# Performance work log

Hardware: AMD Instinct MI355X
Metric: run time of the kernel (lower is better)

## Reference

```python
import jax, jax.numpy as jnp
import numpy as np

IMG = 256      # image size implied by 8x8 grid * scale 32
THRE = 0.5
DIS = 4        # img_dislocate_size
B = 64


def _shift_map(s, size, dis):
    # Pixel-level coordinate map for the dislocated half: cell r starts at
    # max(r*s - dis, 0) (the torch while-loop clamps negative coords to 0).
    p = jnp.arange(size)
    base = jnp.maximum((p // s) * s - dis, 0)
    return base + p % s


def _cell_norm(x, g, s):
    # Per-cell (crop) min/max normalization, matching the per-crop
    # (t - min) / (max - min + 1e-5) in HeatMaptoImg.
    b = x.shape[0]
    v = x.reshape(b, 1, g, s, g, s)
    mn = v.min(axis=(3, 5), keepdims=True)
    mx = v.max(axis=(3, 5), keepdims=True)
    return ((v - mn) / (mx - mn + 1e-5)).reshape(b, 1, g * s, g * s)


def setup_inputs() -> dict:
    key = jax.random.key(0)
    ks = jax.random.split(key, 7)
    B2 = 2 * B
    return {
        "img": jax.random.uniform(ks[0], (B, 1, IMG, IMG), jnp.float32),
        "heat8": jax.random.uniform(ks[1], (B2, 1, 8, 8), jnp.float32),
        "heat16": jax.random.uniform(ks[2], (B2, 1, 16, 16), jnp.float32),
        "heat32": jax.random.uniform(ks[3], (B2, 1, 32, 32), jnp.float32),
        "seg8": jax.random.uniform(ks[4], (B2, 1, IMG, IMG), jnp.float32),
        "seg16": jax.random.uniform(ks[5], (B2, 1, IMG, IMG), jnp.float32),
        "seg32": jax.random.uniform(ks[6], (B2, 1, IMG, IMG), jnp.float32),
    }


def reference(img, heat8, heat16, heat32, seg8, seg16, seg32):
    Bv = img.shape[0]
    label = jnp.zeros((Bv, 1, IMG, IMG), img.dtype)
    cnt = jnp.zeros_like(label)
    crops = {}
    # fine grid (scale 8) processed first, matching the reversed loop order
    for heat, seg, g in ((heat32, seg32, 32), (heat16, seg16, 16), (heat8, seg8, 8)):
        s = IMG // g                      # crop / cell size for this scale
        mask = (heat > THRE).astype(img.dtype)          # (2B,1,g,g)
        mask_pix = jnp.repeat(jnp.repeat(mask, s, axis=2), s, axis=3)  # (2B,1,256,256)
        Y = _shift_map(s, IMG, DIS)
        # dislocated half crops come from the shifted image region
        img_d = img[:, :, Y[:, None], Y[None, :]]       # (B,1,256,256)
        both = jnp.concatenate([img, img_d], axis=0)    # (2B,1,256,256)
        crops[g] = _cell_norm(both, g, s) * mask_pix
        # UnitLabels: scatter-add per-crop labels + counts, then average
        ca = mask_pix[:Bv]
        label = label + ca * seg[:Bv]
        cnt = cnt + ca
        cd = mask_pix[Bv:]
        label = label.at[:, :, Y[:, None], Y[None, :]].add(cd * seg[Bv:])
        cnt = cnt.at[:, :, Y[:, None], Y[None, :]].add(cd)
    label = label / (cnt + 1e-10)
    return (crops[32], crops[16], crops[8], label)
```

## Files before the change

### kernel.cpp

```cpp
#include <hip/hip_runtime.h>

#define IMG   256
#define IMG2  65536
#define NB    64
#define NB2   128

template <int S>
__global__ __launch_bounds__(256) void crops2_kernel(
    const float* __restrict__ img,
    const float* __restrict__ heat,
    float* __restrict__ out) {
    constexpr int G     = IMG / S;
    constexpr int LOG2S = (S == 8) ? 3 : (S == 16) ? 4 : 5;
    constexpr int ROWS  = S + 4;

    __shared__ float tile[ROWS][IMG];
    __shared__ float cAmn[G], cAinv[G], cBmn[G], cBinv[G];

    const int src = blockIdx.y;
    const int ci  = blockIdx.x;
    const int tid = threadIdx.x;

    const int stage_base = (ci == 0) ? 0 : ci * S - 4;
    const float4* img4 = (const float4*)(img + src * IMG2 + stage_base * IMG);

#pragma unroll
    for (int idx = tid; idx < ROWS * 64; idx += 256) {
        const float4 v = img4[idx];
        const int r  = idx >> 6;
        const int c4 = (idx & 63) * 4;
        tile[r][c4 + 0] = v.x;
        tile[r][c4 + 1] = v.y;
        tile[r][c4 + 2] = v.z;
        tile[r][c4 + 3] = v.w;
    }
    __syncthreads();

    const int rA0  = (ci == 0) ? 0 : 4;
    const int cj   = tid >> LOG2S;
    const int colB = (tid < S) ? tid : tid - 4;

    float mnA = 3.4e38f, mxA = -3.4e38f, mnB = 3.4e38f, mxB = -3.4e38f;
#pragma unroll
    for (int r = 0; r < S; ++r) {
        const float a = tile[rA0 + r][tid];
        mnA = fminf(mnA, a); mxA = fmaxf(mxA, a);
        const float bv = tile[r][colB];
        mnB = fminf(mnB, bv); mxB = fmaxf(mxB, bv);
    }
#pragma unroll
    for (int off = 1; off < S; off <<= 1) {
        mnA = fminf(mnA, __shfl_xor(mnA, off, 64));
        mxA = fmaxf(mxA, __shfl_xor(mxA, off, 64));
        mnB = fminf(mnB, __shfl_xor(mnB, off, 64));
        mxB = fmaxf(mxB, __shfl_xor(mxB, off, 64));
    }
    if ((tid & (S - 1)) == 0) {
        const float hA = heat[src * G * G + ci * G + cj];
        const float hB = heat[(src + NB) * G * G + ci * G + cj];
        cAmn[cj]  = mnA;
        cAinv[cj] = (hA > 0.5f ? 1.0f : 0.0f) / (mxA - mnA + 1e-5f);
        cBmn[cj]  = mnB;
        cBinv[cj] = (hB > 0.5f ? 1.0f : 0.0f) / (mxB - mnB + 1e-5f);
    }
    __syncthreads();

    float4* outA = (float4*)(out + src * IMG2 + ci * S * IMG);
    float4* outB = (float4*)(out + (src + NB) * IMG2 + ci * S * IMG);
#pragma unroll
    for (int idx = tid; idx < S * 64; idx += 256) {
        const int r  = idx >> 6;
        const int c0 = (idx & 63) * 4;
        const int cc = c0 >> LOG2S;
        {
            const float mn = cAmn[cc], inv = cAinv[cc];
            float4 o;
            o.x = (tile[rA0 + r][c0 + 0] - mn) * inv;
            o.y = (tile[rA0 + r][c0 + 1] - mn) * inv;
            o.z = (tile[rA0 + r][c0 + 2] - mn) * inv;
            o.w = (tile[rA0 + r][c0 + 3] - mn) * inv;
            outA[idx] = o;
        }
        {
            const float mn = cBmn[cc], inv = cBinv[cc];
            const int gb = (c0 < S) ? c0 : c0 - 4;
            float4 o;
            o.x = (tile[r][gb + 0] - mn) * inv;
            o.y = (tile[r][gb + 1] - mn) * inv;
            o.z = (tile[r][gb + 2] - mn) * inv;
            o.w = (tile[r][gb + 3] - mn) * inv;
            outB[idx] = o;
        }
    }
}

__global__ __launch_bounds__(256) void label2_kernel(
    const float* __restrict__ heat8,
    const float* __restrict__ heat16,
    const float* __restrict__ heat32,
    const float* __restrict__ seg8,
    const float* __restrict__ seg16,
    const float* __restrict__ seg32,
    float* __restrict__ out) {
    const int b = blockIdx.y;
    const int u = blockIdx.x;
    const int v = threadIdx.x;

    float num = 0.0f, den = 0.0f;

    if (u >= 32 && u <= 251) {
        const int i1 = u + 4;
        const int j1 = min(v + 4, 255);
#define SCALE_FAST(heat, seg, g, l, s)                                        \
        {                                                                     \
            const float* __restrict__ h1 = heat + b * (g * g);                \
            const float* __restrict__ h2 = heat + (NB + b) * (g * g);         \
            const float* __restrict__ s1 = seg + b * IMG2;                    \
            const float* __restrict__ s2 = seg + (NB + b) * IMG2;             \
            const float hd  = h1[(u >> l) * g + (v >> l)];                    \
            const float sd  = s1[u * IMG + v];                                \
            const float hg0 = h2[(i1 >> l) * g + (v >> l)];                   \
            const float hg1 = h2[(i1 >> l) * g + (j1 >> l)];                  \
            const float sg0 = s2[i1 * IMG + v];                               \
            const float sg1 = s2[i1 * IMG + j1];                              \
            const float md = (hd > 0.5f) ? 1.0f : 0.0f;                       \
            const float m0 = (v < (s) && hg0 > 0.5f) ? 1.0f : 0.0f;           \
            const float m1 = (v >= (s) - 4 && v <= 251 && hg1 > 0.5f)         \
                                 ? 1.0f : 0.0f;                               \
            num = fmaf(md, sd, num);                                          \
            num = fmaf(m0, sg0, num);                                         \
            num = fmaf(m1, sg1, num);                                         \
            den += md + m0 + m1;                                              \
        }
        SCALE_FAST(heat32, seg32, 32, 3, 8)
        SCALE_FAST(heat16, seg16, 16, 4, 16)
        SCALE_FAST(heat8,  seg8,  8,  5, 32)
#undef SCALE_FAST
    } else {
        const int i0 = u, i1 = min(u + 4, 255);
        const int j0 = v, j1 = min(v + 4, 255);
#define SCALE_GEN(heat, seg, g, l, s)                                         \
        {                                                                     \
            const float* __restrict__ h1 = heat + b * (g * g);                \
            const float* __restrict__ h2 = heat + (NB + b) * (g * g);         \
            const float* __restrict__ s1 = seg + b * IMG2;                    \
            const float* __restrict__ s2 = seg + (NB + b) * IMG2;             \
            const float miA = (u < (s)) ? 1.0f : 0.0f;                        \
            const float miB = (u >= (s) - 4 && u <= 251) ? 1.0f : 0.0f;       \
            const float mjA = (v < (s)) ? 1.0f : 0.0f;                        \
            const float mjB = (v >= (s) - 4 && v <= 251) ? 1.0f : 0.0f;       \
            const float hd  = h1[(u >> l) * g + (v >> l)];                    \
            const float sd  = s1[u * IMG + v];                                \
            const float h00 = h2[(i0 >> l) * g + (j0 >> l)];                  \
            const float h01 = h2[(i0 >> l) * g + (j1 >> l)];                  \
            const float h10 = h2[(i1 >> l) * g + (j0 >> l)];                  \
            const float h11 = h2[(i1 >> l) * g + (j1 >> l)];                  \
            const float s00 = s2[i0 * IMG + j0];                              \
            const float s01 = s2[i0 * IMG + j1];                              \
            const float s10 = s2[i1 * IMG + j0];                              \
            const float s11 = s2[i1 * IMG + j1];                              \
            const float md  = (hd > 0.5f) ? 1.0f : 0.0f;                      \
            const float m00 = (h00 > 0.5f) ? miA * mjA : 0.0f;                \
            const float m01 = (h01 > 0.5f) ? miA * mjB : 0.0f;                \
            const float m10 = (h10 > 0.5f) ? miB * mjA : 0.0f;                \
            const float m11 = (h11 > 0.5f) ? miB * mjB : 0.0f;                \
            num = fmaf(md, sd, num);                                          \
            num = fmaf(m00, s00, num);                                        \
            num = fmaf(m01, s01, num);                                        \
            num = fmaf(m10, s10, num);                                        \
            num = fmaf(m11, s11, num);                                        \
            den += md + m00 + m01 + m10 + m11;                                \
        }
        SCALE_GEN(heat32, seg32, 32, 3, 8)
        SCALE_GEN(heat16, seg16, 16, 4, 16)
        SCALE_GEN(heat8,  seg8,  8,  5, 32)
#undef SCALE_GEN
    }

    out[b * IMG2 + u * IMG + v] = num / (den + 1e-10f);
}

extern "C" void kernel_launch(void* const* d_in, const int* in_sizes, int n_in,
                              void* d_out, int out_size, void* d_ws, size_t ws_size,
                              hipStream_t stream) {
    const float* img    = (const float*)d_in[0];
    const float* heat8  = (const float*)d_in[1];
    const float* heat16 = (const float*)d_in[2];
    const float* heat32 = (const float*)d_in[3];
    const float* seg8   = (const float*)d_in[4];
    const float* seg16  = (const float*)d_in[5];
    const float* seg32  = (const float*)d_in[6];

    float* out     = (float*)d_out;
    float* crops32 = out;
    float* crops16 = out + (size_t)NB2 * IMG2;
    float* crops8  = out + (size_t)2 * NB2 * IMG2;
    float* label   = out + (size_t)3 * NB2 * IMG2;

    crops2_kernel<8><<<dim3(32, NB), 256, 0, stream>>>(img, heat32, crops32);
    crops2_kernel<16><<<dim3(16, NB), 256, 0, stream>>>(img, heat16, crops16);
    crops2_kernel<32><<<dim3(8, NB), 256, 0, stream>>>(img, heat8, crops8);

    label2_kernel<<<dim3(IMG, NB), 256, 0, stream>>>(
        heat8, heat16, heat32, seg8, seg16, seg32, label);
}
```

Measured before the change: 229.7 us.

## Fuse crop and label kernels into one launch with register-based crop normalization

Merges the three per-scale crop kernels and the label kernel into a single launch, with the block index choosing the work type. The crop path no longer stages a row band in a large shared-memory tile. Each thread reads float4s straight from global memory, reduces min/max through shuffles and a small shared cross-wave table, then re-reads the image to write normalized outputs. This removes launch gaps and the big LDS footprint, which should help occupancy. The cost is reading the image twice and branch divergence only at block level.

```diff
diff --git a/kernel.cpp b/kernel.cpp
--- a/kernel.cpp
+++ b/kernel.cpp
@@ -5,107 +5,107 @@
 #define NB    64
 #define NB2   128
 
+#define NBLK_C8   2048
+#define NBLK_C16  1024
+#define NBLK_C32  512
+#define NBLK_LBL  16384
+#define NBLK_ALL  (NBLK_C8 + NBLK_C16 + NBLK_C32 + NBLK_LBL)
+
 template <int S>
-__global__ __launch_bounds__(256) void crops2_kernel(
+__device__ __forceinline__ void crops_cell_row(
     const float* __restrict__ img,
     const float* __restrict__ heat,
-    float* __restrict__ out) {
-    constexpr int G     = IMG / S;
-    constexpr int LOG2S = (S == 8) ? 3 : (S == 16) ? 4 : 5;
-    constexpr int ROWS  = S + 4;
-
-    __shared__ float tile[ROWS][IMG];
-    __shared__ float cAmn[G], cAinv[G], cBmn[G], cBinv[G];
-
-    const int src = blockIdx.y;
-    const int ci  = blockIdx.x;
+    float* __restrict__ out,
+    int src, int ci,
+    float (*s_red)[32][4],
+    float (*s_fin)[4]) {
+    constexpr int G   = IMG / S;
+    constexpr int L   = (S == 8) ? 3 : (S == 16) ? 4 : 5;
+    constexpr int CPL = S / 4;
+
     const int tid = threadIdx.x;
-
-    const int stage_base = (ci == 0) ? 0 : ci * S - 4;
-    const float4* img4 = (const float4*)(img + src * IMG2 + stage_base * IMG);
-
-#pragma unroll
-    for (int idx = tid; idx < ROWS * 64; idx += 256) {
-        const float4 v = img4[idx];
-        const int r  = idx >> 6;
-        const int c4 = (idx & 63) * 4;
-        tile[r][c4 + 0] = v.x;
-        tile[r][c4 + 1] = v.y;
-        tile[r][c4 + 2] = v.z;
-        tile[r][c4 + 3] = v.w;
-    }
-    __syncthreads();
-
-    const int rA0  = (ci == 0) ? 0 : 4;
-    const int cj   = tid >> LOG2S;
-    const int colB = (tid < S) ? tid : tid - 4;
+    const int w   = tid >> 6;
+    const int l   = tid & 63;
+    const int cj  = l >> (L - 2);
+    const int o   = (l & (CPL - 1)) * 4;
+
+    const int rA   = ci * S;
+    const int rB   = (ci == 0) ? 0 : rA - 4;
+    const int colA = cj * S + o;
+    const int colB = ((cj == 0) ? 0 : cj * S - 4) + o;
+
+    const float* __restrict__ sp = img + (size_t)src * IMG2;
 
     float mnA = 3.4e38f, mxA = -3.4e38f, mnB = 3.4e38f, mxB = -3.4e38f;
 #pragma unroll
-    for (int r = 0; r < S; ++r) {
-        const float a = tile[rA0 + r][tid];
-        mnA = fminf(mnA, a); mxA = fmaxf(mxA, a);
-        const float bv = tile[r][colB];
-        mnB = fminf(mnB, bv); mxB = fmaxf(mxB, bv);
-    }
-#pragma unroll
-    for (int off = 1; off < S; off <<= 1) {
+    for (int k = 0; k < S / 4; ++k) {
+        const int r = w + 4 * k;
+        const float4 a = *(const float4*)(sp + (rA + r) * IMG + colA);
+        const float4 bq = *(const float4*)(sp + (rB + r) * IMG + colB);
+        mnA = fminf(mnA, fminf(fminf(a.x, a.y), fminf(a.z, a.w)));
+        mxA = fmaxf(mxA, fmaxf(fmaxf(a.x, a.y), fmaxf(a.z, a.w)));
+        mnB = fminf(mnB, fminf(fminf(bq.x, bq.y), fminf(bq.z, bq.w)));
+        mxB = fmaxf(mxB, fmaxf(fmaxf(bq.x, bq.y), fmaxf(bq.z, bq.w)));
+    }
+#pragma unroll
+    for (int off = 1; off < CPL; off <<= 1) {
         mnA = fminf(mnA, __shfl_xor(mnA, off, 64));
         mxA = fmaxf(mxA, __shfl_xor(mxA, off, 64));
         mnB = fminf(mnB, __shfl_xor(mnB, off, 64));
         mxB = fmaxf(mxB, __shfl_xor(mxB, off, 64));
     }
-    if ((tid & (S - 1)) == 0) {
-        const float hA = heat[src * G * G + ci * G + cj];
-        const float hB = heat[(src + NB) * G * G + ci * G + cj];
-        cAmn[cj]  = mnA;
-        cAinv[cj] = (hA > 0.5f ? 1.0f : 0.0f) / (mxA - mnA + 1e-5f);
-        cBmn[cj]  = mnB;
-        cBinv[cj] = (hB > 0.5f ? 1.0f : 0.0f) / (mxB - mnB + 1e-5f);
+    if ((l & (CPL - 1)) == 0) {
+        float* p = &s_red[w][cj][0];
+        p[0] = mnA; p[1] = mxA; p[2] = mnB; p[3] = mxB;
     }
     __syncthreads();
-
-    float4* outA = (float4*)(out + src * IMG2 + ci * S * IMG);
-    float4* outB = (float4*)(out + (src + NB) * IMG2 + ci * S * IMG);
-#pragma unroll
-    for (int idx = tid; idx < S * 64; idx += 256) {
-        const int r  = idx >> 6;
-        const int c0 = (idx & 63) * 4;
-        const int cc = c0 >> LOG2S;
-        {
-            const float mn = cAmn[cc], inv = cAinv[cc];
-            float4 o;
-            o.x = (tile[rA0 + r][c0 + 0] - mn) * inv;
-            o.y = (tile[rA0 + r][c0 + 1] - mn) * inv;
-            o.z = (tile[rA0 + r][c0 + 2] - mn) * inv;
-            o.w = (tile[rA0 + r][c0 + 3] - mn) * inv;
-            outA[idx] = o;
+    if (tid < G) {
+        float a0 = 3.4e38f, a1 = -3.4e38f, b0 = 3.4e38f, b1 = -3.4e38f;
+#pragma unroll
+        for (int ww = 0; ww < 4; ++ww) {
+            a0 = fminf(a0, s_red[ww][tid][0]);
+            a1 = fmaxf(a1, s_red[ww][tid][1]);
+            b0 = fminf(b0, s_red[ww][tid][2]);
+            b1 = fmaxf(b1, s_red[ww][tid][3]);
         }
-        {
-            const float mn = cBmn[cc], inv = cBinv[cc];
-            const int gb = (c0 < S) ? c0 : c0 - 4;
-            float4 o;
-            o.x = (tile[r][gb + 0] - mn) * inv;
-            o.y = (tile[r][gb + 1] - mn) * inv;
-            o.z = (tile[r][gb + 2] - mn) * inv;
-            o.w = (tile[r][gb + 3] - mn) * inv;
-            outB[idx] = o;
-        }
-    }
-}
-
-__global__ __launch_bounds__(256) void label2_kernel(
+        const float hA = heat[(size_t)src * G * G + ci * G + tid];
+        const float hB = heat[(size_t)(src + NB) * G * G + ci * G + tid];
+        s_fin[tid][0] = a0;
+        s_fin[tid][1] = (hA > 0.5f ? 1.0f : 0.0f) / (a1 - a0 + 1e-5f);
+        s_fin[tid][2] = b0;
+        s_fin[tid][3] = (hB > 0.5f ? 1.0f : 0.0f) / (b1 - b0 + 1e-5f);
+    }
+    __syncthreads();
+    const float fmnA = s_fin[cj][0], finvA = s_fin[cj][1];
+    const float fmnB = s_fin[cj][2], finvB = s_fin[cj][3];
+
+    float* __restrict__ dA = out + (size_t)src * IMG2;
+    float* __restrict__ dB = out + (size_t)(src + NB) * IMG2;
+#pragma unroll
+    for (int k = 0; k < S / 4; ++k) {
+        const int r = w + 4 * k;
+        const float4 a = *(const float4*)(sp + (rA + r) * IMG + colA);
+        const float4 bq = *(const float4*)(sp + (rB + r) * IMG + colB);
+        float4 oa, ob;
+        oa.x = (a.x - fmnA) * finvA;  oa.y = (a.y - fmnA) * finvA;
+        oa.z = (a.z - fmnA) * finvA;  oa.w = (a.w - fmnA) * finvA;
+        ob.x = (bq.x - fmnB) * finvB; ob.y = (bq.y - fmnB) * finvB;
+        ob.z = (bq.z - fmnB) * finvB; ob.w = (bq.w - fmnB) * finvB;
+        *(float4*)(dA + (rA + r) * IMG + colA) = oa;
+        *(float4*)(dB + (rA + r) * IMG + colA) = ob;
+    }
+}
+
+__device__ __forceinline__ void label_pixel_row(
     const float* __restrict__ heat8,
     const float* __restrict__ heat16,
     const float* __restrict__ heat32,
     const float* __restrict__ seg8,
     const float* __restrict__ seg16,
     const float* __restrict__ seg32,
-    float* __restrict__ out) {
-    const int b = blockIdx.y;
-    const int u = blockIdx.x;
+    float* __restrict__ out,
+    int b, int u) {
     const int v = threadIdx.x;
-
     float num = 0.0f, den = 0.0f;
 
     if (u >= 32 && u <= 251) {
@@ -177,7 +177,40 @@
 #undef SCALE_GEN
     }
 
-    out[b * IMG2 + u * IMG + v] = num / (den + 1e-10f);
+    out[(size_t)b * IMG2 + u * IMG + v] = num / (den + 1e-10f);
+}
+
+__global__ __launch_bounds__(256) void fused_kernel(
+    const float* __restrict__ img,
+    const float* __restrict__ heat8,
+    const float* __restrict__ heat16,
+    const float* __restrict__ heat32,
+    const float* __restrict__ seg8,
+    const float* __restrict__ seg16,
+    const float* __restrict__ seg32,
+    float* __restrict__ out) {
+    __shared__ float s_red[4][32][4];
+    __shared__ float s_fin[32][4];
+
+    float* crops32 = out;
+    float* crops16 = out + (size_t)NB2 * IMG2;
+    float* crops8  = out + (size_t)2 * NB2 * IMG2;
+    float* label   = out + (size_t)3 * NB2 * IMG2;
+
+    const int bid = blockIdx.x;
+    if (bid < NBLK_C8) {
+        crops_cell_row<8>(img, heat32, crops32, bid >> 5, bid & 31, s_red, s_fin);
+    } else if (bid < NBLK_C8 + NBLK_C16) {
+        const int t = bid - NBLK_C8;
+        crops_cell_row<16>(img, heat16, crops16, t >> 4, t & 15, s_red, s_fin);
+    } else if (bid < NBLK_C8 + NBLK_C16 + NBLK_C32) {
+        const int t = bid - (NBLK_C8 + NBLK_C16);
+        crops_cell_row<32>(img, heat8, crops8, t >> 3, t & 7, s_red, s_fin);
+    } else {
+        const int t = bid - (NBLK_C8 + NBLK_C16 + NBLK_C32);
+        label_pixel_row(heat8, heat16, heat32, seg8, seg16, seg32, label,
+                        t >> 8, t & 255);
+    }
 }
 
 extern "C" void kernel_launch(void* const* d_in, const int* in_sizes, int n_in,
@@ -191,16 +224,6 @@
     const float* seg16  = (const float*)d_in[5];
     const float* seg32  = (const float*)d_in[6];
 
-    float* out     = (float*)d_out;
-    float* crops32 = out;
-    float* crops16 = out + (size_t)NB2 * IMG2;
-    float* crops8  = out + (size_t)2 * NB2 * IMG2;
-    float* label   = out + (size_t)3 * NB2 * IMG2;
-
-    crops2_kernel<8><<<dim3(32, NB), 256, 0, stream>>>(img, heat32, crops32);
-    crops2_kernel<16><<<dim3(16, NB), 256, 0, stream>>>(img, heat16, crops16);
-    crops2_kernel<32><<<dim3(8, NB), 256, 0, stream>>>(img, heat8, crops8);
-
-    label2_kernel<<<dim3(IMG, NB), 256, 0, stream>>>(
-        heat8, heat16, heat32, seg8, seg16, seg32, label);
-}
+    fused_kernel<<<dim3(NBLK_ALL), 256, 0, stream>>>(
+        img, heat8, heat16, heat32, seg8, seg16, seg32, (float*)d_out);
+}
```

Result: no change. 230.6 us (+0.4%).
